# Optimization experiments

Hardware: AMD Instinct MI355X
Metric: run time of the kernel (lower is better)

The kernel has to match this reference:

```python
import jax, jax.numpy as jnp
import numpy as np

N_NODES = 50000


def gcn_layer(x, W, b, src, dst, norm):
    # x: [N, Fin] -> [N, Fout]; PyG GCNConv: x' = D^-1/2 (A+I) D^-1/2 (x W) + b
    h = x @ W
    msg = h[src] * norm[:, None]              # gather + scale per edge (incl. self loops)
    out = jax.ops.segment_sum(msg, dst, num_segments=N_NODES)
    return out + b


def setup_inputs() -> dict:
    key = jax.random.key(0)
    ks = jax.random.split(key, 12)
    F_in, F_hid, T, E = 128, 128, 10, 1600000
    features = jax.random.normal(ks[0], (N_NODES, F_in), dtype=jnp.float32)
    edges = jax.random.randint(ks[1], (2, E), 0, N_NODES, dtype=jnp.int64)
    s = 1.0 / np.sqrt(F_in)
    W0 = jax.random.uniform(ks[2], (F_in, F_hid), jnp.float32, -s, s)
    b0 = jnp.zeros((F_hid,), jnp.float32)
    W1 = jax.random.uniform(ks[3], (F_hid, F_hid), jnp.float32, -s, s)
    b1 = jnp.zeros((F_hid,), jnp.float32)
    W2 = jax.random.uniform(ks[4], (F_hid, F_hid), jnp.float32, -s, s)
    b2 = jnp.zeros((F_hid,), jnp.float32)
    Wout = jax.random.uniform(ks[5], (F_hid, T), jnp.float32, -s, s)
    bout = jax.random.uniform(ks[6], (T,), jnp.float32, -s, s)
    return {"features": features, "edges": edges, "W0": W0, "b0": b0,
            "W1": W1, "b1": b1, "W2": W2, "b2": b2, "Wout": Wout, "bout": bout}


def reference(features, edges, W0, b0, W1, b1, W2, b2, Wout, bout):
    # Add self loops once; edge structure shared across layers.
    loop = jnp.arange(N_NODES, dtype=edges.dtype)
    src = jnp.concatenate([edges[0], loop])
    dst = jnp.concatenate([edges[1], loop])
    deg = jax.ops.segment_sum(jnp.ones_like(dst, dtype=features.dtype), dst,
                              num_segments=N_NODES)
    dinv = jnp.where(deg > 0, jax.lax.rsqrt(deg), 0.0)
    norm = dinv[src] * dinv[dst]              # [E + N]

    x = gcn_layer(features, W0, b0, src, dst, norm)
    x = gcn_layer(x, W1, b1, src, dst, norm)
    x = gcn_layer(x, W2, b2, src, dst, norm)

    pooled = jnp.mean(x, axis=0)              # [F_hid]
    logits = pooled @ Wout + bout             # [T]
    return jax.nn.log_softmax(logits, axis=0).reshape(1, -1)
```

## Files before the change

### kernel.cpp

```cpp
#include <hip/hip_runtime.h>


#define FDIM 128
#define HSZ 12500
#define NBG 64
#define BSZ 196
#define NBKT 256
#define SCB 256
#define STG 6400


__global__ void __launch_bounds__(256)
count_kernel(const int* __restrict__ edges, int E, int e4,
             int* __restrict__ blockCnt) {
  __shared__ int cnt[NBKT];
  for (int i = threadIdx.x; i < NBKT; i += 256) cnt[i] = 0;
  __syncthreads();
  const int per4 = (e4 + SCB - 1) / SCB;
  const int i0 = blockIdx.x * per4;
  const int i1 = min(e4, i0 + per4);
  const int4* s4 = (const int4*)edges;
  for (int i = i0 + threadIdx.x; i < i1; i += 256) {
    int4 s = s4[i];
    atomicAdd(&cnt[s.x / BSZ], 1);
    atomicAdd(&cnt[s.y / BSZ], 1);
    atomicAdd(&cnt[s.z / BSZ], 1);
    atomicAdd(&cnt[s.w / BSZ], 1);
  }
  if (blockIdx.x == 0) {
    for (int e = 4 * e4 + threadIdx.x; e < E; e += 256)
      atomicAdd(&cnt[edges[e] / BSZ], 1);
  }
  __syncthreads();
  for (int i = threadIdx.x; i < NBKT; i += 256)
    blockCnt[blockIdx.x * NBKT + i] = cnt[i];
}

__global__ void __launch_bounds__(256)
scanA_kernel(const int* __restrict__ blockCnt, int* __restrict__ blockOff,
             int* __restrict__ meta) {
  const int k = blockIdx.x * 4 + (threadIdx.x >> 6);
  const int lane = threadIdx.x & 63;
  int v[4];
  int s = 0;
  #pragma unroll
  for (int i = 0; i < 4; ++i) {
    v[i] = blockCnt[(lane * 4 + i) * NBKT + k];
    s += v[i];
  }
  int inc = s;
  #pragma unroll
  for (int o = 1; o < 64; o <<= 1) {
    int t = __shfl_up(inc, o, 64);
    if (lane >= o) inc += t;
  }
  int run = inc - s;
  #pragma unroll
  for (int i = 0; i < 4; ++i) {
    blockOff[(lane * 4 + i) * NBKT + k] = run;
    run += v[i];
  }
  if (lane == 63) meta[NBKT + k] = inc;
}

__global__ void __launch_bounds__(256)
scanB_kernel(int* __restrict__ meta) {
  __shared__ int wsum[4];
  const int t = threadIdx.x;
  const int lane = t & 63, wv = t >> 6;
  int x = meta[NBKT + t];
  int inc = x;
  #pragma unroll
  for (int o = 1; o < 64; o <<= 1) {
    int q = __shfl_up(inc, o, 64);
    if (lane >= o) inc += q;
  }
  if (lane == 63) wsum[wv] = inc;
  __syncthreads();
  int base = 0;
  for (int w = 0; w < wv; ++w) base += wsum[w];
  meta[t] = base + inc - x;
}

__global__ void __launch_bounds__(256)
scatter_kernel(const int* __restrict__ edges, int E, int e4,
               const int* __restrict__ blockOff, const int* __restrict__ meta,
               int* __restrict__ bucket) {
  __shared__ int cnt[NBKT];
  __shared__ int off2[NBKT];
  __shared__ int offRun[NBKT];
  __shared__ int stg[STG];
  const int per4 = (e4 + SCB - 1) / SCB;
  const int i0 = blockIdx.x * per4;
  const int i1 = min(e4, i0 + per4);
  const int4* s4 = (const int4*)edges;
  const int4* d4 = (const int4*)(edges + E);

  for (int i = threadIdx.x; i < NBKT; i += 256) cnt[i] = 0;
  __syncthreads();
  for (int i = i0 + threadIdx.x; i < i1; i += 256) {
    int4 s = s4[i];
    atomicAdd(&cnt[s.x / BSZ], 1);
    atomicAdd(&cnt[s.y / BSZ], 1);
    atomicAdd(&cnt[s.z / BSZ], 1);
    atomicAdd(&cnt[s.w / BSZ], 1);
  }
  if (blockIdx.x == 0) {
    for (int e = 4 * e4 + threadIdx.x; e < E; e += 256)
      atomicAdd(&cnt[edges[e] / BSZ], 1);
  }
  __syncthreads();
  if (threadIdx.x == 0) {
    int acc = 0;
    for (int q = 0; q < NBKT; ++q) { off2[q] = acc; offRun[q] = acc; acc += cnt[q]; }
  }
  __syncthreads();
  for (int i = i0 + threadIdx.x; i < i1; i += 256) {
    int4 s = s4[i];
    int4 d = d4[i];
    int b, p;
    b = s.x / BSZ; p = atomicAdd(&offRun[b], 1); stg[p] = ((s.x - b * BSZ) << 16) | d.x;
    b = s.y / BSZ; p = atomicAdd(&offRun[b], 1); stg[p] = ((s.y - b * BSZ) << 16) | d.y;
    b = s.z / BSZ; p = atomicAdd(&offRun[b], 1); stg[p] = ((s.z - b * BSZ) << 16) | d.z;
    b = s.w / BSZ; p = atomicAdd(&offRun[b], 1); stg[p] = ((s.w - b * BSZ) << 16) | d.w;
  }
  if (blockIdx.x == 0) {
    for (int e = 4 * e4 + threadIdx.x; e < E; e += 256) {
      int s = edges[e], d = edges[E + e];
      int b = s / BSZ;
      int p = atomicAdd(&offRun[b], 1);
      stg[p] = ((s - b * BSZ) << 16) | d;
    }
  }
  __syncthreads();
  const int wv = threadIdx.x >> 6;
  const int ln = threadIdx.x & 63;
  for (int k = wv; k < NBKT; k += 4) {
    const int len = cnt[k];
    const int lb = off2[k];
    const int gb = meta[k] + blockOff[blockIdx.x * NBKT + k];
    for (int i = ln; i < len; i += 64)
      bucket[gb + i] = stg[lb + i];
  }
}


__global__ void __launch_bounds__(1024)
hist_deg_kernel(const int* __restrict__ edges, int E, int e4, int N,
                int* __restrict__ partial) {
  __shared__ int h[HSZ];
  const int g = blockIdx.x / NBG;
  const int j = blockIdx.x - g * NBG;
  const int lo = g * HSZ;
  const int hi = min(N, lo + HSZ);
  const int hs = hi - lo;
  for (int i = threadIdx.x; i < hs; i += blockDim.x) h[i] = 0;
  __syncthreads();
  const int* dst = edges + E;
  const int4* dst4 = (const int4*)dst;
  for (int i = j * blockDim.x + threadIdx.x; i < e4; i += NBG * blockDim.x) {
    int4 d = dst4[i];
    if (d.x >= lo && d.x < hi) atomicAdd(&h[d.x - lo], 1);
    if (d.y >= lo && d.y < hi) atomicAdd(&h[d.y - lo], 1);
    if (d.z >= lo && d.z < hi) atomicAdd(&h[d.z - lo], 1);
    if (d.w >= lo && d.w < hi) atomicAdd(&h[d.w - lo], 1);
  }
  if (j == 0) {
    for (int e = 4 * e4 + threadIdx.x; e < E; e += blockDim.x) {
      int d = dst[e];
      if (d >= lo && d < hi) atomicAdd(&h[d - lo], 1);
    }
  }
  __syncthreads();
  int* out = partial + (size_t)blockIdx.x * HSZ;
  for (int i = threadIdx.x; i < hs; i += blockDim.x) out[i] = h[i];
}

__global__ void merge_dinv_kernel(const int* __restrict__ partial,
                                  float* __restrict__ dinv, int N) {
  int n = blockIdx.x * blockDim.x + threadIdx.x;
  if (n >= N) return;
  int g = n / HSZ;
  int off = n - g * HSZ;
  const int* p = partial + ((size_t)g * NBG) * HSZ + off;
  int s = 1;
  for (int jj = 0; jj < NBG; ++jj) s += p[(size_t)jj * HSZ];
  dinv[n] = rsqrtf((float)s);
}


__global__ void __launch_bounds__(1024)
pass_kernel(const int* __restrict__ bucket, const int* __restrict__ meta,
            const float* __restrict__ dinv, const float* __restrict__ win,
            float* __restrict__ wout, float* __restrict__ ssump,
            const float* __restrict__ feat, float* __restrict__ v0p,
            int N, int doV0) {
  __shared__ float uacc[16][200];
  __shared__ float ul[BSZ];
  __shared__ float red[16];
  __shared__ float partS[8][FDIM];
  const int t = threadIdx.x;
  const int wv = t >> 6;
  const int b = blockIdx.x;
  const int n0 = b * BSZ;
  const int ns = min(BSZ, N - n0);

  for (int i = t; i < 16 * 200; i += 1024)
    ((float*)uacc)[i] = 0.f;
  __syncthreads();

  const int base = meta[b];
  const int end = base + meta[NBKT + b];
  for (int i = base + t; i < end; i += 1024) {
    int p = bucket[i];
    atomicAdd(&uacc[wv][p >> 16], win[p & 0xFFFF]);
  }
  __syncthreads();

  float u = 0.f;
  if (t < ns) {
    float s = 0.f;
    #pragma unroll
    for (int k = 0; k < 16; ++k) s += uacc[k][t];
    int n = n0 + t;
    u = dinv[n] * (s + win[n]);
    if (wout) wout[n] = dinv[n] * u;
    ul[t] = u;
  } else if (t < BSZ) {
    ul[t] = 0.f;
  }
  if (ssump) {
    float a = u;
    for (int o = 32; o > 0; o >>= 1) a += __shfl_down(a, o, 64);
    if ((t & 63) == 0) red[wv] = a;
    __syncthreads();
    if (t == 0) {
      float s = 0.f;
      #pragma unroll
      for (int k = 0; k < 16; ++k) s += red[k];
      ssump[b] = s;
    }
  }
  if (doV0) {
    __syncthreads();
    const int f = t & (FDIM - 1);
    const int r8 = t >> 7;
    float acc = 0.f;
    for (int r = r8; r < ns; r += 8)
      acc += ul[r] * feat[(size_t)(n0 + r) * FDIM + f];
    partS[r8][f] = acc;
    __syncthreads();
    if (r8 == 0) {
      float s = 0.f;
      #pragma unroll
      for (int k = 0; k < 8; ++k) s += partS[k][f];
      v0p[(size_t)b * FDIM + f] = s;
    }
  }
}


__global__ void __launch_bounds__(1024)
final_kernel(const float* __restrict__ W0, const float* __restrict__ b0,
             const float* __restrict__ W1, const float* __restrict__ b1,
             const float* __restrict__ W2, const float* __restrict__ b2,
             const float* __restrict__ Wout, const float* __restrict__ bout,
             const float* __restrict__ v0p, int nv0,
             const float* __restrict__ ssumpA,
             const float* __restrict__ ssumpB,
             int nss,
             float* __restrict__ out, int N) {
  __shared__ float Wl[FDIM * FDIM];
  __shared__ float WoL[FDIM * 10];
  __shared__ float va[FDIM], vb[FDIM];
  __shared__ float part[8][FDIM];
  __shared__ float red0[16], red1[16];
  __shared__ float shS1, shS2;
  __shared__ float lg[10];
  const int t = threadIdx.x;
  const int f = t & (FDIM - 1);
  const int sl = t >> 7;

  {
    const float4* w4 = (const float4*)W0;
    float4* l4 = (float4*)Wl;
    #pragma unroll
    for (int i = 0; i < 4; ++i) l4[t + i * 1024] = w4[t + i * 1024];
    if (t < (FDIM * 10) / 4) ((float4*)WoL)[t] = ((const float4*)Wout)[t];
  }
  float acc = 0.f;
  for (int j = sl; j < nv0; j += 8) acc += v0p[(size_t)j * FDIM + f];
  part[sl][f] = acc;
  {
    float a0 = 0.f, a1 = 0.f;
    for (int j = t; j < nss; j += 1024) { a0 += ssumpA[j]; a1 += ssumpB[j]; }
    for (int o = 32; o > 0; o >>= 1) {
      a0 += __shfl_down(a0, o, 64);
      a1 += __shfl_down(a1, o, 64);
    }
    if ((t & 63) == 0) { red0[t >> 6] = a0; red1[t >> 6] = a1; }
  }
  __syncthreads();
  if (sl == 0) {
    float s = 0.f;
    #pragma unroll
    for (int j = 0; j < 8; ++j) s += part[j][f];
    va[f] = s;
  }
  if (t == 0) {
    float x = 0.f, y = 0.f;
    #pragma unroll
    for (int i = 0; i < 16; ++i) { x += red0[i]; y += red1[i]; }
    shS2 = x; shS1 = y;
  }
  __syncthreads();

  acc = 0.f;
  #pragma unroll
  for (int k = 0; k < 16; ++k) {
    int kk = sl * 16 + k;
    acc += va[kk] * Wl[kk * FDIM + f];
  }
  part[sl][f] = acc;
  __syncthreads();
  {
    const float4* w4 = (const float4*)W1;
    float4* l4 = (float4*)Wl;
    #pragma unroll
    for (int i = 0; i < 4; ++i) l4[t + i * 1024] = w4[t + i * 1024];
  }
  if (sl == 0) {
    float s = 0.f;
    #pragma unroll
    for (int j = 0; j < 8; ++j) s += part[j][f];
    vb[f] = s + shS1 * b0[f];
  }
  __syncthreads();

  acc = 0.f;
  #pragma unroll
  for (int k = 0; k < 16; ++k) {
    int kk = sl * 16 + k;
    acc += vb[kk] * Wl[kk * FDIM + f];
  }
  part[sl][f] = acc;
  __syncthreads();
  {
    const float4* w4 = (const float4*)W2;
    float4* l4 = (float4*)Wl;
    #pragma unroll
    for (int i = 0; i < 4; ++i) l4[t + i * 1024] = w4[t + i * 1024];
  }
  if (sl == 0) {
    float s = 0.f;
    #pragma unroll
    for (int j = 0; j < 8; ++j) s += part[j][f];
    va[f] = s + shS2 * b1[f];
  }
  __syncthreads();

  acc = 0.f;
  #pragma unroll
  for (int k = 0; k < 16; ++k) {
    int kk = sl * 16 + k;
    acc += va[kk] * Wl[kk * FDIM + f];
  }
  part[sl][f] = acc;
  __syncthreads();
  if (sl == 0) {
    float s = 0.f;
    #pragma unroll
    for (int j = 0; j < 8; ++j) s += part[j][f];
    vb[f] = s / (float)N + b2[f];
  }
  __syncthreads();

  if (t < 10) {
    float a = 0.f;
    for (int k = 0; k < FDIM; ++k) a += vb[k] * WoL[k * 10 + t];
    lg[t] = a + bout[t];
  }
  __syncthreads();
  if (t == 0) {
    float m = lg[0];
    for (int q = 1; q < 10; ++q) m = fmaxf(m, lg[q]);
    float s = 0.f;
    for (int q = 0; q < 10; ++q) s += expf(lg[q] - m);
    float lse = logf(s);
    for (int q = 0; q < 10; ++q) out[q] = lg[q] - m - lse;
  }
}


__global__ void __launch_bounds__(1024)
hist_u_kernel(const int* __restrict__ edges, int E, int e4, int N,
              const float* __restrict__ w,
              float* __restrict__ partial) {
  __shared__ float h[HSZ];
  const int g = blockIdx.x / NBG;
  const int j = blockIdx.x - g * NBG;
  const int lo = g * HSZ;
  const int hi = min(N, lo + HSZ);
  const int hs = hi - lo;
  for (int i = threadIdx.x; i < hs; i += blockDim.x) h[i] = 0.f;
  __syncthreads();
  const int4* s4 = (const int4*)edges;
  const int4* d4 = (const int4*)(edges + E);
  for (int i = j * blockDim.x + threadIdx.x; i < e4; i += NBG * blockDim.x) {
    int4 s = s4[i];
    int4 d = d4[i];
    if (s.x >= lo && s.x < hi) atomicAdd(&h[s.x - lo], w[d.x]);
    if (s.y >= lo && s.y < hi) atomicAdd(&h[s.y - lo], w[d.y]);
    if (s.z >= lo && s.z < hi) atomicAdd(&h[s.z - lo], w[d.z]);
    if (s.w >= lo && s.w < hi) atomicAdd(&h[s.w - lo], w[d.w]);
  }
  if (j == 0) {
    const int* se = edges; const int* de = edges + E;
    for (int e = 4 * e4 + threadIdx.x; e < E; e += blockDim.x) {
      int s = se[e], d = de[e];
      if (s >= lo && s < hi) atomicAdd(&h[s - lo], w[d]);
    }
  }
  __syncthreads();
  float* out = partial + (size_t)blockIdx.x * HSZ;
  for (int i = threadIdx.x; i < hs; i += blockDim.x) out[i] = h[i];
}

__global__ void __launch_bounds__(256)
merge_u_kernel(const float* __restrict__ partial,
               const float* __restrict__ dinv,
               const float* __restrict__ win,
               float* __restrict__ uout,
               float* __restrict__ wout,
               float* __restrict__ ssump, int N) {
  __shared__ float red[4];
  int n = blockIdx.x * blockDim.x + threadIdx.x;
  float u = 0.f;
  if (n < N) {
    int g = n / HSZ;
    int off = n - g * HSZ;
    const float* p = partial + ((size_t)g * NBG) * HSZ + off;
    float s = 0.f;
    for (int jj = 0; jj < NBG; ++jj) s += p[(size_t)jj * HSZ];
    u = dinv[n] * (s + win[n]);
    if (uout) uout[n] = u;
    if (wout) wout[n] = dinv[n] * u;
  }
  if (ssump) {
    float a = u;
    for (int o = 32; o > 0; o >>= 1) a += __shfl_down(a, o, 64);
    if ((threadIdx.x & 63) == 0) red[threadIdx.x >> 6] = a;
    __syncthreads();
    if (threadIdx.x == 0)
      ssump[blockIdx.x] = red[0] + red[1] + red[2] + red[3];
  }
}

__global__ void __launch_bounds__(1024)
v0_kernel(const float* __restrict__ feat, const float* __restrict__ u0,
          float* __restrict__ v0p, int N) {
  __shared__ float sh[8][FDIM];
  int f = threadIdx.x & (FDIM - 1);
  int r8 = threadIdx.x >> 7;
  float acc = 0.f;
  for (int r = blockIdx.x * 8 + r8; r < N; r += 128 * 8)
    acc += u0[r] * feat[(size_t)r * FDIM + f];
  sh[r8][f] = acc;
  __syncthreads();
  if (r8 == 0) {
    float s = acc;
    #pragma unroll
    for (int k = 1; k < 8; ++k) s += sh[k][f];
    v0p[(size_t)blockIdx.x * FDIM + f] = s;
  }
}


extern "C" void kernel_launch(void* const* d_in, const int* in_sizes, int n_in,
                              void* d_out, int out_size, void* d_ws, size_t ws_size,
                              hipStream_t stream) {
  const float* feat = (const float*)d_in[0];
  const int*   edges = (const int*)d_in[1];
  const float* W0 = (const float*)d_in[2];
  const float* b0 = (const float*)d_in[3];
  const float* W1 = (const float*)d_in[4];
  const float* b1 = (const float*)d_in[5];
  const float* W2 = (const float*)d_in[6];
  const float* b2 = (const float*)d_in[7];
  const float* Wout = (const float*)d_in[8];
  const float* bout = (const float*)d_in[9];

  const int N = in_sizes[0] / FDIM;
  const int E = in_sizes[1] / 2;
  const int e4 = E >> 2;
  const int mergeGrid = (N + 255) / 256;

  char* ws = (char*)d_ws;
  size_t nb = ((size_t)N * 4 + 511) & ~(size_t)511;
  size_t partB = ((size_t)4 * NBG * HSZ * 4 + 511) & ~(size_t)511;
  size_t v0pB = ((size_t)NBKT * FDIM * 4 + 511) & ~(size_t)511;
  size_t ssBsz = ((size_t)NBKT * 4 + 511) & ~(size_t)511;
  size_t bktB = ((size_t)E * 4 + 511) & ~(size_t)511;
  size_t cntB = (size_t)SCB * NBKT * 4;
  size_t need = partB + 4 * nb + v0pB + 2 * ssBsz + bktB + 2 * cntB + 4096;

  char* p = ws;
  float* part = (float*)p;       p += partB;
  float* dinv = (float*)p;       p += nb;
  float* w2   = (float*)p;       p += nb;
  float* w1   = (float*)p;       p += nb;
  float* u0   = (float*)p;       p += nb;
  float* v0p  = (float*)p;       p += v0pB;
  float* ssA  = (float*)p;       p += ssBsz;
  float* ssB_ = (float*)p;       p += ssBsz;
  int* bucket = (int*)p;         p += bktB;
  int* blockCnt = (int*)p;       p += cntB;
  int* blockOff = (int*)p;       p += cntB;
  int* meta   = (int*)p;

  const int perBlkEdges = ((e4 + SCB - 1) / SCB) * 4 + 4;
  const bool bucketOK = (ws_size >= need) && (N <= NBKT * BSZ) &&
                        (N <= 65535) && (perBlkEdges <= STG) && ((E & 3) == 0);

  if (bucketOK) {
    count_kernel<<<SCB, 256, 0, stream>>>(edges, E, e4, blockCnt);
    scanA_kernel<<<NBKT / 4, 256, 0, stream>>>(blockCnt, blockOff, meta);
    scanB_kernel<<<1, NBKT, 0, stream>>>(meta);
    scatter_kernel<<<SCB, 256, 0, stream>>>(edges, E, e4, blockOff, meta, bucket);
    hist_deg_kernel<<<4 * NBG, 1024, 0, stream>>>(edges, E, e4, N, (int*)part);
    merge_dinv_kernel<<<mergeGrid, 256, 0, stream>>>((const int*)part, dinv, N);
    pass_kernel<<<NBKT, 1024, 0, stream>>>(bucket, meta, dinv, dinv,
                                           w2, ssA, nullptr, nullptr, N, 0);
    pass_kernel<<<NBKT, 1024, 0, stream>>>(bucket, meta, dinv, w2,
                                           w1, ssB_, nullptr, nullptr, N, 0);
    pass_kernel<<<NBKT, 1024, 0, stream>>>(bucket, meta, dinv, w1,
                                           nullptr, nullptr, feat, v0p, N, 1);
    final_kernel<<<1, 1024, 0, stream>>>(W0, b0, W1, b1, W2, b2, Wout, bout,
                                         v0p, NBKT, ssA, ssB_, NBKT,
                                         (float*)d_out, N);
  } else {
    hist_deg_kernel<<<4 * NBG, 1024, 0, stream>>>(edges, E, e4, N, (int*)part);
    merge_dinv_kernel<<<mergeGrid, 256, 0, stream>>>((const int*)part, dinv, N);
    hist_u_kernel<<<4 * NBG, 1024, 0, stream>>>(edges, E, e4, N, dinv, part);
    merge_u_kernel<<<mergeGrid, 256, 0, stream>>>(part, dinv, dinv,
                                                  nullptr, w2, ssA, N);
    hist_u_kernel<<<4 * NBG, 1024, 0, stream>>>(edges, E, e4, N, w2, part);
    merge_u_kernel<<<mergeGrid, 256, 0, stream>>>(part, dinv, w2,
                                                  nullptr, w1, ssB_, N);
    hist_u_kernel<<<4 * NBG, 1024, 0, stream>>>(edges, E, e4, N, w1, part);
    merge_u_kernel<<<mergeGrid, 256, 0, stream>>>(part, dinv, w1,
                                                  u0, nullptr, nullptr, N);
    v0_kernel<<<128, 1024, 0, stream>>>(feat, u0, v0p, N);
    final_kernel<<<1, 1024, 0, stream>>>(W0, b0, W1, b1, W2, b2, Wout, bout,
                                         v0p, 128, ssA, ssB_, mergeGrid,
                                         (float*)d_out, N);
  }
}
```

Before: 106.7 us.

## Fuse preprocessing kernels: count with degree histogram, scan/scatter with dinv merge

```diff
diff --git a/kernel.cpp b/kernel.cpp
--- a/kernel.cpp
+++ b/kernel.cpp
@@ -10,66 +10,96 @@
 #define STG 6400
 
 
-__global__ void __launch_bounds__(256)
-count_kernel(const int* __restrict__ edges, int E, int e4,
-             int* __restrict__ blockCnt) {
+__global__ void __launch_bounds__(1024)
+k1_count_deg(const int* __restrict__ edges, int E, int e4, int N,
+             int* __restrict__ blockCnt, int* __restrict__ partial) {
+  __shared__ int h[HSZ];
   __shared__ int cnt[NBKT];
-  for (int i = threadIdx.x; i < NBKT; i += 256) cnt[i] = 0;
-  __syncthreads();
+  const int t = threadIdx.x;
+  const int bid = blockIdx.x;
+  const int g = bid >> 6, j = bid & (NBG - 1);
+  const int lo = g * HSZ;
+  const int hi = min(N, lo + HSZ);
+  const int hs = hi - lo;
+  for (int i = t; i < hs; i += 1024) h[i] = 0;
+  if (t < NBKT) cnt[t] = 0;
+  __syncthreads();
+
   const int per4 = (e4 + SCB - 1) / SCB;
-  const int i0 = blockIdx.x * per4;
+  const int i0 = bid * per4;
   const int i1 = min(e4, i0 + per4);
   const int4* s4 = (const int4*)edges;
-  for (int i = i0 + threadIdx.x; i < i1; i += 256) {
+  for (int i = i0 + t; i < i1; i += 1024) {
     int4 s = s4[i];
     atomicAdd(&cnt[s.x / BSZ], 1);
     atomicAdd(&cnt[s.y / BSZ], 1);
     atomicAdd(&cnt[s.z / BSZ], 1);
     atomicAdd(&cnt[s.w / BSZ], 1);
   }
-  if (blockIdx.x == 0) {
-    for (int e = 4 * e4 + threadIdx.x; e < E; e += 256)
+  if (bid == 0) {
+    for (int e = 4 * e4 + t; e < E; e += 1024)
       atomicAdd(&cnt[edges[e] / BSZ], 1);
   }
-  __syncthreads();
-  for (int i = threadIdx.x; i < NBKT; i += 256)
-    blockCnt[blockIdx.x * NBKT + i] = cnt[i];
-}
+
+  const int4* d4 = (const int4*)(edges + E);
+  for (int i = j * 1024 + t; i < e4; i += NBG * 1024) {
+    int4 d = d4[i];
+    if (d.x >= lo && d.x < hi) atomicAdd(&h[d.x - lo], 1);
+    if (d.y >= lo && d.y < hi) atomicAdd(&h[d.y - lo], 1);
+    if (d.z >= lo && d.z < hi) atomicAdd(&h[d.z - lo], 1);
+    if (d.w >= lo && d.w < hi) atomicAdd(&h[d.w - lo], 1);
+  }
+  if (j == 0) {
+    const int* dst = edges + E;
+    for (int e = 4 * e4 + t; e < E; e += 1024) {
+      int d = dst[e];
+      if (d >= lo && d < hi) atomicAdd(&h[d - lo], 1);
+    }
+  }
+  __syncthreads();
+  if (t < NBKT) blockCnt[bid * NBKT + t] = cnt[t];
+  int* op = partial + (size_t)bid * HSZ;
+  for (int i = t; i < hs; i += 1024) op[i] = h[i];
+}
+
 
 __global__ void __launch_bounds__(256)
-scanA_kernel(const int* __restrict__ blockCnt, int* __restrict__ blockOff,
-             int* __restrict__ meta) {
-  const int k = blockIdx.x * 4 + (threadIdx.x >> 6);
-  const int lane = threadIdx.x & 63;
-  int v[4];
-  int s = 0;
-  #pragma unroll
-  for (int i = 0; i < 4; ++i) {
-    v[i] = blockCnt[(lane * 4 + i) * NBKT + k];
-    s += v[i];
-  }
-  int inc = s;
-  #pragma unroll
-  for (int o = 1; o < 64; o <<= 1) {
-    int t = __shfl_up(inc, o, 64);
-    if (lane >= o) inc += t;
-  }
-  int run = inc - s;
-  #pragma unroll
-  for (int i = 0; i < 4; ++i) {
-    blockOff[(lane * 4 + i) * NBKT + k] = run;
-    run += v[i];
-  }
-  if (lane == 63) meta[NBKT + k] = inc;
-}
-
-__global__ void __launch_bounds__(256)
-scanB_kernel(int* __restrict__ meta) {
+k2_scatter_dinv(const int* __restrict__ edges, int E, int e4, int N,
+                const int* __restrict__ blockCnt,
+                const int* __restrict__ partial,
+                int* __restrict__ bucket, int* __restrict__ meta,
+                float* __restrict__ dinv) {
+  const int bid = blockIdx.x;
+  const int t = threadIdx.x;
+
+  if (bid >= SCB) {
+    int n = (bid - SCB) * 256 + t;
+    if (n < N) {
+      int gg = n / HSZ, off = n - gg * HSZ;
+      const int* p = partial + ((size_t)gg * NBG) * HSZ + off;
+      int s = 1;
+      for (int jj = 0; jj < NBG; ++jj) s += p[(size_t)jj * HSZ];
+      dinv[n] = rsqrtf((float)s);
+    }
+    return;
+  }
+
+  __shared__ int baseS[NBKT];
+  __shared__ int off2[NBKT];
+  __shared__ int offRun[NBKT];
+  __shared__ int cntS[NBKT];
   __shared__ int wsum[4];
-  const int t = threadIdx.x;
+  __shared__ int stg[STG];
+
   const int lane = t & 63, wv = t >> 6;
-  int x = meta[NBKT + t];
-  int inc = x;
+  const int myCnt = blockCnt[bid * NBKT + t];
+  int myoff = 0, total = 0;
+  for (int b = 0; b < SCB; ++b) {
+    int v = blockCnt[b * NBKT + t];
+    if (b < bid) myoff += v;
+    total += v;
+  }
+  int inc = total;
   #pragma unroll
   for (int o = 1; o < 64; o <<= 1) {
     int q = __shfl_up(inc, o, 64);
@@ -77,45 +107,33 @@
   }
   if (lane == 63) wsum[wv] = inc;
   __syncthreads();
-  int base = 0;
-  for (int w = 0; w < wv; ++w) base += wsum[w];
-  meta[t] = base + inc - x;
-}
-
-__global__ void __launch_bounds__(256)
-scatter_kernel(const int* __restrict__ edges, int E, int e4,
-               const int* __restrict__ blockOff, const int* __restrict__ meta,
-               int* __restrict__ bucket) {
-  __shared__ int cnt[NBKT];
-  __shared__ int off2[NBKT];
-  __shared__ int offRun[NBKT];
-  __shared__ int stg[STG];
+  int wb = 0;
+  for (int w = 0; w < wv; ++w) wb += wsum[w];
+  const int gbase = wb + inc - total;
+  baseS[t] = gbase + myoff;
+  if (bid == 0) { meta[t] = gbase; meta[NBKT + t] = total; }
+  int inc2 = myCnt;
+  #pragma unroll
+  for (int o = 1; o < 64; o <<= 1) {
+    int q = __shfl_up(inc2, o, 64);
+    if (lane >= o) inc2 += q;
+  }
+  __syncthreads();
+  if (lane == 63) wsum[wv] = inc2;
+  __syncthreads();
+  int wb2 = 0;
+  for (int w = 0; w < wv; ++w) wb2 += wsum[w];
+  off2[t] = wb2 + inc2 - myCnt;
+  offRun[t] = off2[t];
+  cntS[t] = myCnt;
+  __syncthreads();
+
   const int per4 = (e4 + SCB - 1) / SCB;
-  const int i0 = blockIdx.x * per4;
+  const int i0 = bid * per4;
   const int i1 = min(e4, i0 + per4);
   const int4* s4 = (const int4*)edges;
   const int4* d4 = (const int4*)(edges + E);
-
-  for (int i = threadIdx.x; i < NBKT; i += 256) cnt[i] = 0;
-  __syncthreads();
-  for (int i = i0 + threadIdx.x; i < i1; i += 256) {
-    int4 s = s4[i];
-    atomicAdd(&cnt[s.x / BSZ], 1);
-    atomicAdd(&cnt[s.y / BSZ], 1);
-    atomicAdd(&cnt[s.z / BSZ], 1);
-    atomicAdd(&cnt[s.w / BSZ], 1);
-  }
-  if (blockIdx.x == 0) {
-    for (int e = 4 * e4 + threadIdx.x; e < E; e += 256)
-      atomicAdd(&cnt[edges[e] / BSZ], 1);
-  }
-  __syncthreads();
-  if (threadIdx.x == 0) {
-    int acc = 0;
-    for (int q = 0; q < NBKT; ++q) { off2[q] = acc; offRun[q] = acc; acc += cnt[q]; }
-  }
-  __syncthreads();
-  for (int i = i0 + threadIdx.x; i < i1; i += 256) {
+  for (int i = i0 + t; i < i1; i += 256) {
     int4 s = s4[i];
     int4 d = d4[i];
     int b, p;
@@ -124,8 +142,8 @@
     b = s.z / BSZ; p = atomicAdd(&offRun[b], 1); stg[p] = ((s.z - b * BSZ) << 16) | d.z;
     b = s.w / BSZ; p = atomicAdd(&offRun[b], 1); stg[p] = ((s.w - b * BSZ) << 16) | d.w;
   }
-  if (blockIdx.x == 0) {
-    for (int e = 4 * e4 + threadIdx.x; e < E; e += 256) {
+  if (bid == 0) {
+    for (int e = 4 * e4 + t; e < E; e += 256) {
       int s = edges[e], d = edges[E + e];
       int b = s / BSZ;
       int p = atomicAdd(&offRun[b], 1);
@@ -133,59 +151,13 @@
     }
   }
   __syncthreads();
-  const int wv = threadIdx.x >> 6;
-  const int ln = threadIdx.x & 63;
   for (int k = wv; k < NBKT; k += 4) {
-    const int len = cnt[k];
+    const int len = cntS[k];
     const int lb = off2[k];
-    const int gb = meta[k] + blockOff[blockIdx.x * NBKT + k];
-    for (int i = ln; i < len; i += 64)
+    const int gb = baseS[k];
+    for (int i = lane; i < len; i += 64)
       bucket[gb + i] = stg[lb + i];
   }
-}
-
-
-__global__ void __launch_bounds__(1024)
-hist_deg_kernel(const int* __restrict__ edges, int E, int e4, int N,
-                int* __restrict__ partial) {
-  __shared__ int h[HSZ];
-  const int g = blockIdx.x / NBG;
-  const int j = blockIdx.x - g * NBG;
-  const int lo = g * HSZ;
-  const int hi = min(N, lo + HSZ);
-  const int hs = hi - lo;
-  for (int i = threadIdx.x; i < hs; i += blockDim.x) h[i] = 0;
-  __syncthreads();
-  const int* dst = edges + E;
-  const int4* dst4 = (const int4*)dst;
-  for (int i = j * blockDim.x + threadIdx.x; i < e4; i += NBG * blockDim.x) {
-    int4 d = dst4[i];
-    if (d.x >= lo && d.x < hi) atomicAdd(&h[d.x - lo], 1);
-    if (d.y >= lo && d.y < hi) atomicAdd(&h[d.y - lo], 1);
-    if (d.z >= lo && d.z < hi) atomicAdd(&h[d.z - lo], 1);
-    if (d.w >= lo && d.w < hi) atomicAdd(&h[d.w - lo], 1);
-  }
-  if (j == 0) {
-    for (int e = 4 * e4 + threadIdx.x; e < E; e += blockDim.x) {
-      int d = dst[e];
-      if (d >= lo && d < hi) atomicAdd(&h[d - lo], 1);
-    }
-  }
-  __syncthreads();
-  int* out = partial + (size_t)blockIdx.x * HSZ;
-  for (int i = threadIdx.x; i < hs; i += blockDim.x) out[i] = h[i];
-}
-
-__global__ void merge_dinv_kernel(const int* __restrict__ partial,
-                                  float* __restrict__ dinv, int N) {
-  int n = blockIdx.x * blockDim.x + threadIdx.x;
-  if (n >= N) return;
-  int g = n / HSZ;
-  int off = n - g * HSZ;
-  const int* p = partial + ((size_t)g * NBG) * HSZ + off;
-  int s = 1;
-  for (int jj = 0; jj < NBG; ++jj) s += p[(size_t)jj * HSZ];
-  dinv[n] = rsqrtf((float)s);
 }
 
 
@@ -393,6 +365,49 @@
 
 
 __global__ void __launch_bounds__(1024)
+hist_deg_kernel(const int* __restrict__ edges, int E, int e4, int N,
+                int* __restrict__ partial) {
+  __shared__ int h[HSZ];
+  const int g = blockIdx.x / NBG;
+  const int j = blockIdx.x - g * NBG;
+  const int lo = g * HSZ;
+  const int hi = min(N, lo + HSZ);
+  const int hs = hi - lo;
+  for (int i = threadIdx.x; i < hs; i += blockDim.x) h[i] = 0;
+  __syncthreads();
+  const int* dst = edges + E;
+  const int4* dst4 = (const int4*)dst;
+  for (int i = j * blockDim.x + threadIdx.x; i < e4; i += NBG * blockDim.x) {
+    int4 d = dst4[i];
+    if (d.x >= lo && d.x < hi) atomicAdd(&h[d.x - lo], 1);
+    if (d.y >= lo && d.y < hi) atomicAdd(&h[d.y - lo], 1);
+    if (d.z >= lo && d.z < hi) atomicAdd(&h[d.z - lo], 1);
+    if (d.w >= lo && d.w < hi) atomicAdd(&h[d.w - lo], 1);
+  }
+  if (j == 0) {
+    for (int e = 4 * e4 + threadIdx.x; e < E; e += blockDim.x) {
+      int d = dst[e];
+      if (d >= lo && d < hi) atomicAdd(&h[d - lo], 1);
+    }
+  }
+  __syncthreads();
+  int* out = partial + (size_t)blockIdx.x * HSZ;
+  for (int i = threadIdx.x; i < hs; i += blockDim.x) out[i] = h[i];
+}
+
+__global__ void merge_dinv_kernel(const int* __restrict__ partial,
+                                  float* __restrict__ dinv, int N) {
+  int n = blockIdx.x * blockDim.x + threadIdx.x;
+  if (n >= N) return;
+  int g = n / HSZ;
+  int off = n - g * HSZ;
+  const int* p = partial + ((size_t)g * NBG) * HSZ + off;
+  int s = 1;
+  for (int jj = 0; jj < NBG; ++jj) s += p[(size_t)jj * HSZ];
+  dinv[n] = rsqrtf((float)s);
+}
+
+__global__ void __launch_bounds__(1024)
 hist_u_kernel(const int* __restrict__ edges, int E, int e4, int N,
               const float* __restrict__ w,
               float* __restrict__ partial) {
@@ -502,7 +517,7 @@
   size_t ssBsz = ((size_t)NBKT * 4 + 511) & ~(size_t)511;
   size_t bktB = ((size_t)E * 4 + 511) & ~(size_t)511;
   size_t cntB = (size_t)SCB * NBKT * 4;
-  size_t need = partB + 4 * nb + v0pB + 2 * ssBsz + bktB + 2 * cntB + 4096;
+  size_t need = partB + 4 * nb + v0pB + 2 * ssBsz + bktB + cntB + 4096;
 
   char* p = ws;
   float* part = (float*)p;       p += partB;
@@ -515,7 +530,6 @@
   float* ssB_ = (float*)p;       p += ssBsz;
   int* bucket = (int*)p;         p += bktB;
   int* blockCnt = (int*)p;       p += cntB;
-  int* blockOff = (int*)p;       p += cntB;
   int* meta   = (int*)p;
 
   const int perBlkEdges = ((e4 + SCB - 1) / SCB) * 4 + 4;
@@ -523,12 +537,10 @@
                         (N <= 65535) && (perBlkEdges <= STG) && ((E & 3) == 0);
 
   if (bucketOK) {
-    count_kernel<<<SCB, 256, 0, stream>>>(edges, E, e4, blockCnt);
-    scanA_kernel<<<NBKT / 4, 256, 0, stream>>>(blockCnt, blockOff, meta);
-    scanB_kernel<<<1, NBKT, 0, stream>>>(meta);
-    scatter_kernel<<<SCB, 256, 0, stream>>>(edges, E, e4, blockOff, meta, bucket);
-    hist_deg_kernel<<<4 * NBG, 1024, 0, stream>>>(edges, E, e4, N, (int*)part);
-    merge_dinv_kernel<<<mergeGrid, 256, 0, stream>>>((const int*)part, dinv, N);
+    k1_count_deg<<<SCB, 1024, 0, stream>>>(edges, E, e4, N,
+                                           blockCnt, (int*)part);
+    k2_scatter_dinv<<<SCB + mergeGrid, 256, 0, stream>>>(
+        edges, E, e4, N, blockCnt, (const int*)part, bucket, meta, dinv);
     pass_kernel<<<NBKT, 1024, 0, stream>>>(bucket, meta, dinv, dinv,
                                            w2, ssA, nullptr, nullptr, N, 0);
     pass_kernel<<<NBKT, 1024, 0, stream>>>(bucket, meta, dinv, w2,
```

Result: faster. 101.9 us (-4.5%).
